# Optimization experiments

Measured on AMD Instinct MI355X. Metric: run time of the kernel, lower is better.

The kernel has to match this reference:

```python
import jax, jax.numpy as jnp
import numpy as np

NUM_HEADS = 8
HEAD_DIM = 64  # hidden_dim // num_heads = 512 // 8
THRESHOLD = 0.5


def setup_inputs() -> dict:
    key = jax.random.key(0)
    ks = jax.random.split(key, 12)
    B, T, D, Hd = 4, 1024, 512, 512
    s = 0.02
    inp = {
        'x': jax.random.normal(ks[0], (B, T, D), dtype=jnp.float32),
        'Wq': jax.random.normal(ks[1], (D, Hd), dtype=jnp.float32) * s,
        'bq': jnp.zeros((Hd,), jnp.float32),
        'Wk': jax.random.normal(ks[2], (D, Hd), dtype=jnp.float32) * s,
        'bk': jnp.zeros((Hd,), jnp.float32),
        'Wv': jax.random.normal(ks[3], (D, Hd), dtype=jnp.float32) * s,
        'bv': jnp.zeros((Hd,), jnp.float32),
        'conv_w': jax.random.normal(ks[4], (NUM_HEADS,), dtype=jnp.float32) * 0.3,
        'conv_b': jnp.zeros((1,), jnp.float32),
        'Wfh': jax.random.normal(ks[5], (Hd, Hd), dtype=jnp.float32) * s,
        'bfh': jnp.zeros((Hd,), jnp.float32),
        'Wfg': jax.random.normal(ks[6], (Hd, Hd), dtype=jnp.float32) * s,
        'bfg': jnp.zeros((Hd,), jnp.float32),
        'Wrh': jax.random.normal(ks[7], (Hd, Hd), dtype=jnp.float32) * s,
        'brh': jnp.zeros((Hd,), jnp.float32),
        'Wrg': jax.random.normal(ks[8], (Hd, Hd), dtype=jnp.float32) * s,
        'brg': jnp.zeros((Hd,), jnp.float32),
    }
    return inp


def reference(x, Wq, bq, Wk, bk, Wv, bv, conv_w, conv_b,
              Wfh, bfh, Wfg, bfg, Wrh, brh, Wrg, brg):
    B, T, D = x.shape
    H, hd = NUM_HEADS, HEAD_DIM
    scale = hd ** -0.5

    q = (x @ Wq + bq).reshape(B, T, H, hd).transpose(0, 2, 1, 3)  # [B,H,T,hd]
    k = (x @ Wk + bk).reshape(B, T, H, hd).transpose(0, 2, 1, 3)
    v = (x @ Wv + bv).reshape(B, T, H, hd).transpose(0, 2, 1, 3)

    scores = jnp.einsum('bhqd,bhkd->bhqk', q, k) * scale        # [B,H,T,T]
    A_t = jax.nn.softmax(scores, axis=-1)

    # cross-head 1x1 conv: weighted sum over heads -> [B,1,T,T]
    R_f = jax.nn.sigmoid(jnp.einsum('bhqk,h->bqk', A_t, conv_w) + conv_b[0])
    R_f = R_f[:, None]                                           # [B,1,T,T]
    M_f = (R_f <= THRESHOLD).astype(A_t.dtype)
    M_r = (1.0 - R_f <= THRESHOLD).astype(A_t.dtype)

    A_f = jax.nn.softmax(A_t * M_f, axis=-1)
    A_r = jax.nn.softmax(A_t * M_r, axis=-1)

    T_f = jnp.einsum('bhqk,bhkd->bhqd', A_f, v).transpose(0, 2, 1, 3).reshape(B, T, H * hd)
    T_r = jnp.einsum('bhqk,bhkd->bhqd', A_r, v).transpose(0, 2, 1, 3).reshape(B, T, H * hd)

    F_f = T_f @ Wfh + bfh
    G_f = jax.nn.sigmoid(T_f @ Wfg + bfg)
    F_r = T_r @ Wrh + brh
    G_r = jax.nn.sigmoid(T_r @ Wrg + brg)

    G_cat = jax.nn.softmax(jnp.stack([G_f, G_r], axis=-1), axis=-1)  # [B,T,Hd,2]
    F_t = F_f * G_cat[..., 0] + F_r * G_cat[..., 1]
    return F_t
```

## Files before the change

### kernel.cpp

```cpp
#include <hip/hip_runtime.h>
#include <hip/hip_bf16.h>
#include <stdint.h>

typedef short bf16x8 __attribute__((ext_vector_type(8)));
typedef float f32x4 __attribute__((ext_vector_type(4)));

__device__ __forceinline__ unsigned short f2bf(float f) {
  union { float f; unsigned int u; } v;
  v.f = f;
  unsigned int u = v.u;
  u = (u + 0x7fffu + ((u >> 16) & 1u)) >> 16;
  return (unsigned short)u;
}

__device__ __forceinline__ unsigned int cvt_pk_bf16(float lo, float hi) {
  unsigned int r;
  asm("v_cvt_pk_bf16_f32 %0, %1, %2" : "=v"(r) : "v"(lo), "v"(hi));
  return r;
}

typedef union { bf16x8 v; unsigned int u[4]; } frag_u;

__device__ __forceinline__ void gload16(const void* g, void* lds) {
  __builtin_amdgcn_global_load_lds(
      (const __attribute__((address_space(1))) unsigned int*)(unsigned long long)g,
      (__attribute__((address_space(3))) unsigned int*)(unsigned long long)(unsigned)(unsigned long long)lds,
      16, 0, 0);
}

__device__ __forceinline__ bf16x8 lds_frag(const unsigned short* t, int row, int ch4q) {
  return *(const bf16x8*)(t + row * 64 + ((ch4q ^ (row & 7)) << 3));
}


__global__ __launch_bounds__(256) void prep_kernel(
    const float* __restrict__ x,
    const float* __restrict__ Wq, const float* __restrict__ Wk, const float* __restrict__ Wv,
    const float* __restrict__ Wfh, const float* __restrict__ Wfg,
    const float* __restrict__ Wrh, const float* __restrict__ Wrg,
    unsigned short* __restrict__ xb, unsigned short* __restrict__ wt) {
  int bid = blockIdx.x;
  int tid = threadIdx.x;
  if (bid < 256) {
    const float4* xi = (const float4*)x;
#pragma unroll
    for (int rep = 0; rep < 8; rep++) {
      int i = bid * 256 + tid + rep * 65536;
      float4 v = xi[i];
      uint2 u;
      u.x = cvt_pk_bf16(v.x, v.y);
      u.y = cvt_pk_bf16(v.z, v.w);
      *(uint2*)&xb[(size_t)i * 4] = u;
    }
  } else {
    __shared__ float tile[64][65];
    int t = bid - 256;
    int mat = t >> 6;
    t &= 63;
    int tr = (t >> 3) * 64, tc = (t & 7) * 64;
    const float* W = (mat == 0) ? Wq : (mat == 1) ? Wk : (mat == 2) ? Wv
                   : (mat == 3) ? Wfh : (mat == 4) ? Wfg : (mat == 5) ? Wrh : Wrg;
    unsigned short* Wt = wt + (size_t)mat * 512 * 512;
    for (int rep = 0; rep < 16; rep++) {
      int idx = rep * 256 + tid;
      int r = idx >> 6, c = idx & 63;
      tile[r][c] = W[(tr + r) * 512 + tc + c];
    }
    __syncthreads();
    for (int rep = 0; rep < 16; rep++) {
      int idx = rep * 256 + tid;
      int r = idx >> 6, c = idx & 63;
      Wt[(tc + r) * 512 + tr + c] = f2bf(tile[c][r]);
    }
  }
}

__global__ __launch_bounds__(256, 2) void qkv_kernel(
    const unsigned short* __restrict__ xb,
    const unsigned short* __restrict__ wtq, const unsigned short* __restrict__ wtk,
    const unsigned short* __restrict__ wtv,
    const float* __restrict__ bq, const float* __restrict__ bk, const float* __restrict__ bv,
    unsigned short* __restrict__ Qfrag, unsigned short* __restrict__ Kfrag,
    unsigned short* __restrict__ Vfrag) {
  __shared__ __attribute__((aligned(16))) unsigned short smem[32768];
  unsigned short* st0 = smem;
  unsigned short* st1 = smem + 4608;
  unsigned short* st2 = smem + 9216;
  const int m0 = blockIdx.y * 64, n0 = blockIdx.x * 64;
  const int tid = threadIdx.x, w = tid >> 6, lane = tid & 63;
  const int c = lane & 15, quad = lane >> 4;
  const int wm = w & 1, wn = w >> 1;
  const int rsel = lane >> 3, csel = lane & 7;
  const int sc = csel ^ rsel;
  const char* Ag  = (const char*)xb  + (size_t)(m0 + w * 16 + rsel) * 1024 + sc * 16;
  const char* Bgq = (const char*)wtq + (size_t)(n0 + w * 16 + rsel) * 1024 + sc * 16;
  const char* Bgk = (const char*)wtk + (size_t)(n0 + w * 16 + rsel) * 1024 + sc * 16;
  const char* Bgv = (const char*)wtv + (size_t)(n0 + w * 16 + rsel) * 1024 + sc * 16;
  const int woff = w * 1024;

  f32x4 acc[3][2][2];
  f32x4 z4 = {0.f, 0.f, 0.f, 0.f};
#pragma unroll
  for (int o = 0; o < 3; o++)
#pragma unroll
    for (int i = 0; i < 2; i++)
#pragma unroll
      for (int j = 0; j < 2; j++) acc[o][i][j] = z4;

  {
    unsigned short* base = smem;
    gload16(Ag, base + woff);              gload16(Ag + 8192, base + woff + 512);
    gload16(Bgq, base + 4096 + woff);      gload16(Bgq + 8192, base + 4096 + woff + 512);
    gload16(Bgk, base + 8192 + woff);      gload16(Bgk + 8192, base + 8192 + woff + 512);
    gload16(Bgv, base + 12288 + woff);     gload16(Bgv + 8192, base + 12288 + woff + 512);
  }
  __syncthreads();

  for (int ks = 0; ks < 8; ks++) {
    unsigned short* cur = smem + (ks & 1) * 16384;
    if (ks < 7) {
      unsigned short* nxt = smem + ((ks + 1) & 1) * 16384;
      const int kb = (ks + 1) * 128;
      gload16(Ag + kb, nxt + woff);          gload16(Ag + kb + 8192, nxt + woff + 512);
      gload16(Bgq + kb, nxt + 4096 + woff);  gload16(Bgq + kb + 8192, nxt + 4096 + woff + 512);
      gload16(Bgk + kb, nxt + 8192 + woff);  gload16(Bgk + kb + 8192, nxt + 8192 + woff + 512);
      gload16(Bgv + kb, nxt + 12288 + woff); gload16(Bgv + kb + 8192, nxt + 12288 + woff + 512);
    }
#pragma unroll
    for (int ch = 0; ch < 2; ch++) {
      const int cq = ch * 4 + quad;
      bf16x8 a0 = lds_frag(cur, wm * 32 + c, cq);
      bf16x8 a1 = lds_frag(cur, wm * 32 + 16 + c, cq);
#pragma unroll
      for (int nt = 0; nt < 2; nt++) {
        const int rb = wn * 32 + nt * 16 + c;
        bf16x8 fq = lds_frag(cur + 4096, rb, cq);
        bf16x8 fk = lds_frag(cur + 8192, rb, cq);
        bf16x8 fv = lds_frag(cur + 12288, rb, cq);
        acc[0][0][nt] = __builtin_amdgcn_mfma_f32_16x16x32_bf16(a0, fq, acc[0][0][nt], 0, 0, 0);
        acc[0][1][nt] = __builtin_amdgcn_mfma_f32_16x16x32_bf16(a1, fq, acc[0][1][nt], 0, 0, 0);
        acc[1][0][nt] = __builtin_amdgcn_mfma_f32_16x16x32_bf16(a0, fk, acc[1][0][nt], 0, 0, 0);
        acc[1][1][nt] = __builtin_amdgcn_mfma_f32_16x16x32_bf16(a1, fk, acc[1][1][nt], 0, 0, 0);
        acc[2][0][nt] = __builtin_amdgcn_mfma_f32_16x16x32_bf16(a0, fv, acc[2][0][nt], 0, 0, 0);
        acc[2][1][nt] = __builtin_amdgcn_mfma_f32_16x16x32_bf16(a1, fv, acc[2][1][nt], 0, 0, 0);
      }
    }
    __syncthreads();
  }

#pragma unroll
  for (int ms = 0; ms < 2; ms++)
#pragma unroll
    for (int nt = 0; nt < 2; nt++) {
      int n_l = wn * 32 + nt * 16 + c;
      int n = n0 + n_l;
      float biasq = bq[n], biask = bk[n], biasv = bv[n];
#pragma unroll
      for (int r = 0; r < 4; r++) {
        int m_l = wm * 32 + ms * 16 + quad * 4 + r;
        st0[m_l * 72 + n_l] = f2bf((acc[0][ms][nt][r] + biasq) * 0.125f);
        st1[m_l * 72 + n_l] = f2bf(acc[1][ms][nt][r] + biask);
        st2[n_l * 72 + m_l] = f2bf(acc[2][ms][nt][r] + biasv);
      }
    }
  __syncthreads();

  {
    const int h = n0 >> 6;
    const int bb = m0 >> 10, t0b = (m0 & 1023) >> 4;
#pragma unroll
    for (int sub = 0; sub < 2; sub++) {
      uint4 vq = *(uint4*)&st0[(w * 16 + c) * 72 + sub * 32 + quad * 8];
      uint4 vk = *(uint4*)&st1[(w * 16 + c) * 72 + sub * 32 + quad * 8];
      size_t base = (size_t)((bb * 64 + t0b + w) * 8192) + h * 1024 + sub * 512 + lane * 8;
      *(uint4*)&Qfrag[base] = vq;
      *(uint4*)&Kfrag[base] = vk;
    }
    const int ktq = t0b + w;
    const int ktp = ktq >> 1, half = ktq & 1;
#pragma unroll
    for (int dm = 0; dm < 4; dm++) {
      uint2 vv = *(uint2*)&st2[(dm * 16 + c) * 72 + w * 16 + quad * 4];
      size_t base = (size_t)(bb * 8 + h) * 65536 + (size_t)(ktp * 4 + dm) * 512
                  + lane * 8 + half * 4;
      *(uint2*)&Vfrag[base] = vv;
    }
  }
}

__global__ __launch_bounds__(512, 2) void attn_kernel(
    const unsigned short* __restrict__ Qfrag, const unsigned short* __restrict__ Kfrag,
    const unsigned short* __restrict__ Vfrag,
    const float* __restrict__ conv_w, const float* __restrict__ conv_b,
    unsigned short* __restrict__ Tfb, unsigned short* __restrict__ Trb) {
  const int b = blockIdx.x, qt = blockIdx.y;
  const int tid = threadIdx.x, w = tid >> 6, lane = tid & 63;
  const int c = lane & 15, quad = lane >> 4;
  __shared__ float zbuf[8][16];
  __shared__ float izbuf[8][16];
  __shared__ __attribute__((aligned(16))) float red[2 * 8 * 4 * 64 * 4];
  __shared__ float zred[2][8][16];

  f32x4 z4 = {0.f, 0.f, 0.f, 0.f};
  const float cb = conv_b[0];
  const size_t qbase = (size_t)((b * 64 + qt) * 8192) + lane * 8;
  const size_t kb0 = (size_t)((b * 64 + w * 8) * 8192) + lane * 8;
  const size_t vb0 = (size_t)(b * 8) * 65536 + lane * 8;

  f32x4 g[8];
#pragma unroll
  for (int j = 0; j < 8; j++) g[j] = {cb, cb, cb, cb};

  for (int h = 0; h < 8; h++) {
    bf16x8 qf0 = *(const bf16x8*)&Qfrag[qbase + h * 1024];
    bf16x8 qf1 = *(const bf16x8*)&Qfrag[qbase + h * 1024 + 512];
    f32x4 p[8];
    float zh = 0.f;
#pragma unroll
    for (int j = 0; j < 8; j++) {
      const size_t kb = kb0 + (size_t)j * 8192 + h * 1024;
      bf16x8 kf0 = *(const bf16x8*)&Kfrag[kb];
      bf16x8 kf1 = *(const bf16x8*)&Kfrag[kb + 512];
      f32x4 s = __builtin_amdgcn_mfma_f32_16x16x32_bf16(kf0, qf0, z4, 0, 0, 0);
      s = __builtin_amdgcn_mfma_f32_16x16x32_bf16(kf1, qf1, s, 0, 0, 0);
      p[j][0] = __expf(s[0]); p[j][1] = __expf(s[1]);
      p[j][2] = __expf(s[2]); p[j][3] = __expf(s[3]);
      zh += (p[j][0] + p[j][1]) + (p[j][2] + p[j][3]);
    }
    zh += __shfl_xor(zh, 16); zh += __shfl_xor(zh, 32);
    __syncthreads();
    if (quad == 0) zbuf[w][c] = zh;
    __syncthreads();
    float Z = ((zbuf[0][c] + zbuf[1][c]) + (zbuf[2][c] + zbuf[3][c]))
            + ((zbuf[4][c] + zbuf[5][c]) + (zbuf[6][c] + zbuf[7][c]));
    const float izq = 1.0f / Z;
    if (w == 0 && quad == 0) izbuf[h][c] = izq;
    const float cwz = conv_w[h] * izq;
#pragma unroll
    for (int j = 0; j < 8; j++) {
      g[j][0] += cwz * p[j][0]; g[j][1] += cwz * p[j][1];
      g[j][2] += cwz * p[j][2]; g[j][3] += cwz * p[j][3];
    }
  }

  unsigned int mmx[4], mmy[4];
#pragma unroll
  for (int t = 0; t < 4; t++) {
    unsigned int p0 = 0, p1 = 0;
#pragma unroll
    for (int r = 0; r < 4; r++) {
      p0 |= ((g[2 * t][r] <= 0.f ? 1u : 0u) | (g[2 * t][r] >= 0.f ? 2u : 0u)) << (8 * r);
      p1 |= ((g[2 * t + 1][r] <= 0.f ? 1u : 0u) | (g[2 * t + 1][r] >= 0.f ? 2u : 0u)) << (8 * r);
    }
    mmx[t] = p0; mmy[t] = p1;
  }
  __syncthreads();

  frag_u ones;
  ones.u[0] = 0x3F803F80u; ones.u[1] = 0x3F803F80u;
  ones.u[2] = 0x3F803F80u; ones.u[3] = 0x3F803F80u;

  const int fr = w >> 2, dmslot = w & 3;
  const size_t tbase = (size_t)(b * 1024 + qt * 16 + c) * 512;
  unsigned short* dstsel = (fr == 0) ? Tfb : Trb;

  for (int h = 0; h < 8; h++) {
    bf16x8 qf0 = *(const bf16x8*)&Qfrag[qbase + h * 1024];
    bf16x8 qf1 = *(const bf16x8*)&Qfrag[qbase + h * 1024 + 512];
    const float iz_h = izbuf[h][c];
    f32x4 accf[4], accr[4];
#pragma unroll
    for (int i = 0; i < 4; i++) { accf[i] = z4; accr[i] = z4; }
    f32x4 zf4 = z4, zr4 = z4;
#pragma unroll
    for (int t = 0; t < 4; t++) {
      const size_t kba = kb0 + (size_t)(2 * t) * 8192 + h * 1024;
      const size_t kbb = kba + 8192;
      bf16x8 ka0 = *(const bf16x8*)&Kfrag[kba];
      bf16x8 ka1 = *(const bf16x8*)&Kfrag[kba + 512];
      bf16x8 kb0f = *(const bf16x8*)&Kfrag[kbb];
      bf16x8 kb1f = *(const bf16x8*)&Kfrag[kbb + 512];
      f32x4 sa = __builtin_amdgcn_mfma_f32_16x16x32_bf16(ka0, qf0, z4, 0, 0, 0);
      sa = __builtin_amdgcn_mfma_f32_16x16x32_bf16(ka1, qf1, sa, 0, 0, 0);
      f32x4 sb = __builtin_amdgcn_mfma_f32_16x16x32_bf16(kb0f, qf0, z4, 0, 0, 0);
      sb = __builtin_amdgcn_mfma_f32_16x16x32_bf16(kb1f, qf1, sb, 0, 0, 0);
      float ea[4], eb[4];
#pragma unroll
      for (int r = 0; r < 4; r++) {
        ea[r] = __expf(__expf(sa[r]) * iz_h);
        eb[r] = __expf(__expf(sb[r]) * iz_h);
      }
      frag_u pF, pR;
      pF.u[0] = cvt_pk_bf16((mmx[t] & 0x1u)       ? ea[0] : 1.f, (mmx[t] & 0x100u)     ? ea[1] : 1.f);
      pF.u[1] = cvt_pk_bf16((mmx[t] & 0x10000u)   ? ea[2] : 1.f, (mmx[t] & 0x1000000u) ? ea[3] : 1.f);
      pF.u[2] = cvt_pk_bf16((mmy[t] & 0x1u)       ? eb[0] : 1.f, (mmy[t] & 0x100u)     ? eb[1] : 1.f);
      pF.u[3] = cvt_pk_bf16((mmy[t] & 0x10000u)   ? eb[2] : 1.f, (mmy[t] & 0x1000000u) ? eb[3] : 1.f);
      pR.u[0] = cvt_pk_bf16((mmx[t] & 0x2u)       ? ea[0] : 1.f, (mmx[t] & 0x200u)     ? ea[1] : 1.f);
      pR.u[1] = cvt_pk_bf16((mmx[t] & 0x20000u)   ? ea[2] : 1.f, (mmx[t] & 0x2000000u) ? ea[3] : 1.f);
      pR.u[2] = cvt_pk_bf16((mmy[t] & 0x2u)       ? eb[0] : 1.f, (mmy[t] & 0x200u)     ? eb[1] : 1.f);
      pR.u[3] = cvt_pk_bf16((mmy[t] & 0x20000u)   ? eb[2] : 1.f, (mmy[t] & 0x2000000u) ? eb[3] : 1.f);
      zf4 = __builtin_amdgcn_mfma_f32_16x16x32_bf16(ones.v, pF.v, zf4, 0, 0, 0);
      zr4 = __builtin_amdgcn_mfma_f32_16x16x32_bf16(ones.v, pR.v, zr4, 0, 0, 0);
      const size_t vbh = vb0 + (size_t)h * 65536 + (size_t)((w * 4 + t) * 4) * 512;
#pragma unroll
      for (int dm = 0; dm < 4; dm++) {
        bf16x8 vf = *(const bf16x8*)&Vfrag[vbh + (size_t)dm * 512];
        accf[dm] = __builtin_amdgcn_mfma_f32_16x16x32_bf16(vf, pF.v, accf[dm], 0, 0, 0);
        accr[dm] = __builtin_amdgcn_mfma_f32_16x16x32_bf16(vf, pR.v, accr[dm], 0, 0, 0);
      }
    }
    __syncthreads();
#pragma unroll
    for (int dm = 0; dm < 4; dm++) {
      *(f32x4*)&red[(((0 * 8 + w) * 4 + dm) * 64 + lane) * 4] = accf[dm];
      *(f32x4*)&red[(((1 * 8 + w) * 4 + dm) * 64 + lane) * 4] = accr[dm];
    }
    if (quad == 0) { zred[0][w][c] = zf4[0]; zred[1][w][c] = zr4[0]; }
    __syncthreads();
    {
      f32x4 o = z4;
#pragma unroll
      for (int w2 = 0; w2 < 8; w2++)
        o += *(const f32x4*)&red[(((fr * 8 + w2) * 4 + dmslot) * 64 + lane) * 4];
      float Zq = 0.f;
#pragma unroll
      for (int w2 = 0; w2 < 8; w2++) Zq += zred[fr][w2][c];
      const float iz = 1.0f / Zq;
      uint2 u;
      u.x = cvt_pk_bf16(o[0] * iz, o[1] * iz);
      u.y = cvt_pk_bf16(o[2] * iz, o[3] * iz);
      *(uint2*)&dstsel[tbase + h * 64 + dmslot * 16 + quad * 4] = u;
    }
  }
}

__global__ __launch_bounds__(256, 4) void final_kernel(
    const unsigned short* __restrict__ Tfb, const unsigned short* __restrict__ Trb,
    const unsigned short* __restrict__ wfh, const unsigned short* __restrict__ wfg,
    const unsigned short* __restrict__ wrh, const unsigned short* __restrict__ wrg,
    const float* __restrict__ bfh, const float* __restrict__ bfg,
    const float* __restrict__ brh, const float* __restrict__ brg,
    float* __restrict__ out) {
  __shared__ __attribute__((aligned(16))) unsigned short smem[16384];
  const int m0 = blockIdx.y * 64, n0 = blockIdx.x * 32;
  const int tid = threadIdx.x, w = tid >> 6, lane = tid & 63;
  const int c = lane & 15, quad = lane >> 4;
  const int wm = w & 1, wn = w >> 1;
  const int rsel = lane >> 3, csel = lane & 7;
  const int sc = csel ^ rsel;
  const char* Agf = (const char*)Tfb + (size_t)(m0 + w * 16 + rsel) * 1024 + sc * 16;
  const char* Agr = (const char*)Trb + (size_t)(m0 + w * 16 + rsel) * 1024 + sc * 16;
  const char* Bg0 = (const char*)wfh + (size_t)(n0 + w * 8 + rsel) * 1024 + sc * 16;
  const char* Bg1 = (const char*)wfg + (size_t)(n0 + w * 8 + rsel) * 1024 + sc * 16;
  const char* Bg2 = (const char*)wrh + (size_t)(n0 + w * 8 + rsel) * 1024 + sc * 16;
  const char* Bg3 = (const char*)wrg + (size_t)(n0 + w * 8 + rsel) * 1024 + sc * 16;
  unsigned short* lAf = smem + w * 1024;
  unsigned short* lAr = smem + 4096 + w * 1024;
  unsigned short* l0 = smem + 8192 + w * 512;
  unsigned short* l1 = smem + 10240 + w * 512;
  unsigned short* l2 = smem + 12288 + w * 512;
  unsigned short* l3 = smem + 14336 + w * 512;

  f32x4 acc[4][2];
  f32x4 z4 = {0.f, 0.f, 0.f, 0.f};
#pragma unroll
  for (int o = 0; o < 4; o++)
#pragma unroll
    for (int m = 0; m < 2; m++) acc[o][m] = z4;

  for (int ks = 0; ks < 8; ks++) {
    if (ks) __syncthreads();
    const int kb = ks * 128;
    gload16(Agf + kb, lAf);  gload16(Agf + kb + 8192, lAf + 512);
    gload16(Agr + kb, lAr);  gload16(Agr + kb + 8192, lAr + 512);
    gload16(Bg0 + kb, l0);
    gload16(Bg1 + kb, l1);
    gload16(Bg2 + kb, l2);
    gload16(Bg3 + kb, l3);
    __syncthreads();
#pragma unroll
    for (int ch = 0; ch < 2; ch++) {
      const int cq = ch * 4 + quad;
      bf16x8 af0 = lds_frag(smem, wm * 32 + c, cq);
      bf16x8 af1 = lds_frag(smem, wm * 32 + 16 + c, cq);
      bf16x8 ar0 = lds_frag(smem + 4096, wm * 32 + c, cq);
      bf16x8 ar1 = lds_frag(smem + 4096, wm * 32 + 16 + c, cq);
      const int rb = wn * 16 + c;
      bf16x8 f0 = lds_frag(smem + 8192, rb, cq);
      bf16x8 f1 = lds_frag(smem + 10240, rb, cq);
      bf16x8 f2 = lds_frag(smem + 12288, rb, cq);
      bf16x8 f3 = lds_frag(smem + 14336, rb, cq);
      acc[0][0] = __builtin_amdgcn_mfma_f32_16x16x32_bf16(af0, f0, acc[0][0], 0, 0, 0);
      acc[0][1] = __builtin_amdgcn_mfma_f32_16x16x32_bf16(af1, f0, acc[0][1], 0, 0, 0);
      acc[1][0] = __builtin_amdgcn_mfma_f32_16x16x32_bf16(af0, f1, acc[1][0], 0, 0, 0);
      acc[1][1] = __builtin_amdgcn_mfma_f32_16x16x32_bf16(af1, f1, acc[1][1], 0, 0, 0);
      acc[2][0] = __builtin_amdgcn_mfma_f32_16x16x32_bf16(ar0, f2, acc[2][0], 0, 0, 0);
      acc[2][1] = __builtin_amdgcn_mfma_f32_16x16x32_bf16(ar1, f2, acc[2][1], 0, 0, 0);
      acc[3][0] = __builtin_amdgcn_mfma_f32_16x16x32_bf16(ar0, f3, acc[3][0], 0, 0, 0);
      acc[3][1] = __builtin_amdgcn_mfma_f32_16x16x32_bf16(ar1, f3, acc[3][1], 0, 0, 0);
    }
  }

  {
    int n = n0 + wn * 16 + c;
    float b0 = bfh[n], b1 = bfg[n], b2 = brh[n], b3 = brg[n];
#pragma unroll
    for (int m = 0; m < 2; m++) {
      int t0 = m0 + wm * 32 + m * 16 + quad * 4;
#pragma unroll
      for (int r = 0; r < 4; r++) {
        int t = t0 + r;
        float Ff = acc[0][m][r] + b0;
        float Gf = 1.0f / (1.0f + __expf(-(acc[1][m][r] + b1)));
        float Fr = acc[2][m][r] + b2;
        float Gr = 1.0f / (1.0f + __expf(-(acc[3][m][r] + b3)));
        float ef = __expf(Gf), er = __expf(Gr);
        out[(size_t)t * 512 + n] = (Ff * ef + Fr * er) / (ef + er);
      }
    }
  }
}

extern "C" void kernel_launch(void* const* d_in, const int* in_sizes, int n_in,
                              void* d_out, int out_size, void* d_ws, size_t ws_size,
                              hipStream_t stream) {
  const float* x   = (const float*)d_in[0];
  const float* Wq  = (const float*)d_in[1];
  const float* bq  = (const float*)d_in[2];
  const float* Wk  = (const float*)d_in[3];
  const float* bk  = (const float*)d_in[4];
  const float* Wv  = (const float*)d_in[5];
  const float* bv  = (const float*)d_in[6];
  const float* cw  = (const float*)d_in[7];
  const float* cb  = (const float*)d_in[8];
  const float* Wfh = (const float*)d_in[9];
  const float* bfh = (const float*)d_in[10];
  const float* Wfg = (const float*)d_in[11];
  const float* bfg = (const float*)d_in[12];
  const float* Wrh = (const float*)d_in[13];
  const float* brh = (const float*)d_in[14];
  const float* Wrg = (const float*)d_in[15];
  const float* brg = (const float*)d_in[16];

  char* ws = (char*)d_ws;
  const size_t MB = 1024 * 1024;
  unsigned short* xb    = (unsigned short*)(ws + 0 * MB);
  unsigned short* Qfrag = (unsigned short*)(ws + 4 * MB);
  unsigned short* Kfrag = (unsigned short*)(ws + 8 * MB);
  unsigned short* Vfrag = (unsigned short*)(ws + 12 * MB);
  unsigned short* Tfb   = (unsigned short*)(ws + 16 * MB);
  unsigned short* Trb   = (unsigned short*)(ws + 20 * MB);
  unsigned short* wt    = (unsigned short*)(ws + 24 * MB);
  const size_t WSZ = 512 * 512;

  prep_kernel<<<704, 256, 0, stream>>>(x, Wq, Wk, Wv, Wfh, Wfg, Wrh, Wrg, xb, wt);
  qkv_kernel<<<dim3(8, 64), 256, 0, stream>>>(xb, wt + 0 * WSZ, wt + 1 * WSZ, wt + 2 * WSZ,
                                              bq, bk, bv, Qfrag, Kfrag, Vfrag);
  attn_kernel<<<dim3(4, 64), 512, 0, stream>>>(Qfrag, Kfrag, Vfrag, cw, cb, Tfb, Trb);
  final_kernel<<<dim3(16, 64), 256, 0, stream>>>(Tfb, Trb, wt + 3 * WSZ, wt + 4 * WSZ,
                                                 wt + 5 * WSZ, wt + 6 * WSZ,
                                                 bfh, bfg, brh, brg, (float*)d_out);
}
```

Before: 171.9 us.

## Halve QKV GEMM M-tile and drop LDS double buffering for higher occupancy

The QKV projection kernel now uses 32-row M tiles instead of 64, doubling the grid to 1024 blocks. It drops the double-buffered LDS prefetch for a single buffer with load-sync-compute stages, shrinking shared memory and raising the launch-bounds occupancy hint from 2 to 4. The epilogue repacking is reworked so each wave handles part of the smaller tile. The intent is more parallelism and latency hiding across the GPU; in exchange, memory-to-compute overlap inside a block is lost and the weight tiles are reloaded twice as often.

```diff
diff --git a/kernel.cpp b/kernel.cpp
--- a/kernel.cpp
+++ b/kernel.cpp
@@ -75,115 +75,103 @@
   }
 }
 
-__global__ __launch_bounds__(256, 2) void qkv_kernel(
+__global__ __launch_bounds__(256, 4) void qkv_kernel(
     const unsigned short* __restrict__ xb,
     const unsigned short* __restrict__ wtq, const unsigned short* __restrict__ wtk,
     const unsigned short* __restrict__ wtv,
     const float* __restrict__ bq, const float* __restrict__ bk, const float* __restrict__ bv,
     unsigned short* __restrict__ Qfrag, unsigned short* __restrict__ Kfrag,
     unsigned short* __restrict__ Vfrag) {
-  __shared__ __attribute__((aligned(16))) unsigned short smem[32768];
+  __shared__ __attribute__((aligned(16))) unsigned short smem[14336];
+  unsigned short* As = smem;
+  unsigned short* Bq = smem + 2048;
+  unsigned short* Bk = smem + 6144;
+  unsigned short* Bv = smem + 10240;
   unsigned short* st0 = smem;
-  unsigned short* st1 = smem + 4608;
-  unsigned short* st2 = smem + 9216;
-  const int m0 = blockIdx.y * 64, n0 = blockIdx.x * 64;
+  unsigned short* st1 = smem + 2304;
+  unsigned short* st2 = smem + 4608;
+  const int m0 = blockIdx.y * 32, n0 = blockIdx.x * 64;
   const int tid = threadIdx.x, w = tid >> 6, lane = tid & 63;
   const int c = lane & 15, quad = lane >> 4;
   const int wm = w & 1, wn = w >> 1;
   const int rsel = lane >> 3, csel = lane & 7;
   const int sc = csel ^ rsel;
-  const char* Ag  = (const char*)xb  + (size_t)(m0 + w * 16 + rsel) * 1024 + sc * 16;
+  const char* Ag  = (const char*)xb  + (size_t)(m0 + w * 8 + rsel) * 1024 + sc * 16;
   const char* Bgq = (const char*)wtq + (size_t)(n0 + w * 16 + rsel) * 1024 + sc * 16;
   const char* Bgk = (const char*)wtk + (size_t)(n0 + w * 16 + rsel) * 1024 + sc * 16;
   const char* Bgv = (const char*)wtv + (size_t)(n0 + w * 16 + rsel) * 1024 + sc * 16;
-  const int woff = w * 1024;
-
-  f32x4 acc[3][2][2];
+  unsigned short* lA = As + w * 512;
+  unsigned short* lQ = Bq + w * 1024;
+  unsigned short* lK = Bk + w * 1024;
+  unsigned short* lV = Bv + w * 1024;
+
+  f32x4 acc[3][2];
   f32x4 z4 = {0.f, 0.f, 0.f, 0.f};
 #pragma unroll
   for (int o = 0; o < 3; o++)
 #pragma unroll
-    for (int i = 0; i < 2; i++)
-#pragma unroll
-      for (int j = 0; j < 2; j++) acc[o][i][j] = z4;
-
-  {
-    unsigned short* base = smem;
-    gload16(Ag, base + woff);              gload16(Ag + 8192, base + woff + 512);
-    gload16(Bgq, base + 4096 + woff);      gload16(Bgq + 8192, base + 4096 + woff + 512);
-    gload16(Bgk, base + 8192 + woff);      gload16(Bgk + 8192, base + 8192 + woff + 512);
-    gload16(Bgv, base + 12288 + woff);     gload16(Bgv + 8192, base + 12288 + woff + 512);
-  }
-  __syncthreads();
+    for (int j = 0; j < 2; j++) acc[o][j] = z4;
 
   for (int ks = 0; ks < 8; ks++) {
-    unsigned short* cur = smem + (ks & 1) * 16384;
-    if (ks < 7) {
-      unsigned short* nxt = smem + ((ks + 1) & 1) * 16384;
-      const int kb = (ks + 1) * 128;
-      gload16(Ag + kb, nxt + woff);          gload16(Ag + kb + 8192, nxt + woff + 512);
-      gload16(Bgq + kb, nxt + 4096 + woff);  gload16(Bgq + kb + 8192, nxt + 4096 + woff + 512);
-      gload16(Bgk + kb, nxt + 8192 + woff);  gload16(Bgk + kb + 8192, nxt + 8192 + woff + 512);
-      gload16(Bgv + kb, nxt + 12288 + woff); gload16(Bgv + kb + 8192, nxt + 12288 + woff + 512);
-    }
+    if (ks) __syncthreads();
+    const int kb = ks * 128;
+    gload16(Ag + kb, lA);
+    gload16(Bgq + kb, lQ);  gload16(Bgq + kb + 8192, lQ + 512);
+    gload16(Bgk + kb, lK);  gload16(Bgk + kb + 8192, lK + 512);
+    gload16(Bgv + kb, lV);  gload16(Bgv + kb + 8192, lV + 512);
+    __syncthreads();
 #pragma unroll
     for (int ch = 0; ch < 2; ch++) {
       const int cq = ch * 4 + quad;
-      bf16x8 a0 = lds_frag(cur, wm * 32 + c, cq);
-      bf16x8 a1 = lds_frag(cur, wm * 32 + 16 + c, cq);
+      bf16x8 a = lds_frag(As, wm * 16 + c, cq);
 #pragma unroll
       for (int nt = 0; nt < 2; nt++) {
         const int rb = wn * 32 + nt * 16 + c;
-        bf16x8 fq = lds_frag(cur + 4096, rb, cq);
-        bf16x8 fk = lds_frag(cur + 8192, rb, cq);
-        bf16x8 fv = lds_frag(cur + 12288, rb, cq);
-        acc[0][0][nt] = __builtin_amdgcn_mfma_f32_16x16x32_bf16(a0, fq, acc[0][0][nt], 0, 0, 0);
-        acc[0][1][nt] = __builtin_amdgcn_mfma_f32_16x16x32_bf16(a1, fq, acc[0][1][nt], 0, 0, 0);
-        acc[1][0][nt] = __builtin_amdgcn_mfma_f32_16x16x32_bf16(a0, fk, acc[1][0][nt], 0, 0, 0);
-        acc[1][1][nt] = __builtin_amdgcn_mfma_f32_16x16x32_bf16(a1, fk, acc[1][1][nt], 0, 0, 0);
-        acc[2][0][nt] = __builtin_amdgcn_mfma_f32_16x16x32_bf16(a0, fv, acc[2][0][nt], 0, 0, 0);
-        acc[2][1][nt] = __builtin_amdgcn_mfma_f32_16x16x32_bf16(a1, fv, acc[2][1][nt], 0, 0, 0);
+        bf16x8 fq = lds_frag(Bq, rb, cq);
+        bf16x8 fk = lds_frag(Bk, rb, cq);
+        bf16x8 fv = lds_frag(Bv, rb, cq);
+        acc[0][nt] = __builtin_amdgcn_mfma_f32_16x16x32_bf16(a, fq, acc[0][nt], 0, 0, 0);
+        acc[1][nt] = __builtin_amdgcn_mfma_f32_16x16x32_bf16(a, fk, acc[1][nt], 0, 0, 0);
+        acc[2][nt] = __builtin_amdgcn_mfma_f32_16x16x32_bf16(a, fv, acc[2][nt], 0, 0, 0);
       }
     }
-    __syncthreads();
-  }
-
-#pragma unroll
-  for (int ms = 0; ms < 2; ms++)
-#pragma unroll
-    for (int nt = 0; nt < 2; nt++) {
-      int n_l = wn * 32 + nt * 16 + c;
-      int n = n0 + n_l;
-      float biasq = bq[n], biask = bk[n], biasv = bv[n];
-#pragma unroll
-      for (int r = 0; r < 4; r++) {
-        int m_l = wm * 32 + ms * 16 + quad * 4 + r;
-        st0[m_l * 72 + n_l] = f2bf((acc[0][ms][nt][r] + biasq) * 0.125f);
-        st1[m_l * 72 + n_l] = f2bf(acc[1][ms][nt][r] + biask);
-        st2[n_l * 72 + m_l] = f2bf(acc[2][ms][nt][r] + biasv);
-      }
-    }
+  }
+  __syncthreads();
+
+#pragma unroll
+  for (int nt = 0; nt < 2; nt++) {
+    int n_l = wn * 32 + nt * 16 + c;
+    int n = n0 + n_l;
+    float biasq = bq[n], biask = bk[n], biasv = bv[n];
+#pragma unroll
+    for (int r = 0; r < 4; r++) {
+      int m_l = wm * 16 + quad * 4 + r;
+      st0[m_l * 72 + n_l] = f2bf((acc[0][nt][r] + biasq) * 0.125f);
+      st1[m_l * 72 + n_l] = f2bf(acc[1][nt][r] + biask);
+      st2[n_l * 40 + m_l] = f2bf(acc[2][nt][r] + biasv);
+    }
+  }
   __syncthreads();
 
   {
     const int h = n0 >> 6;
     const int bb = m0 >> 10, t0b = (m0 & 1023) >> 4;
-#pragma unroll
-    for (int sub = 0; sub < 2; sub++) {
-      uint4 vq = *(uint4*)&st0[(w * 16 + c) * 72 + sub * 32 + quad * 8];
-      uint4 vk = *(uint4*)&st1[(w * 16 + c) * 72 + sub * 32 + quad * 8];
-      size_t base = (size_t)((bb * 64 + t0b + w) * 8192) + h * 1024 + sub * 512 + lane * 8;
-      *(uint4*)&Qfrag[base] = vq;
-      *(uint4*)&Kfrag[base] = vk;
-    }
-    const int ktq = t0b + w;
+    const int tw = w >> 1, sub = w & 1;
+    uint4 vq = *(uint4*)&st0[(tw * 16 + c) * 72 + sub * 32 + quad * 8];
+    uint4 vk = *(uint4*)&st1[(tw * 16 + c) * 72 + sub * 32 + quad * 8];
+    size_t base = (size_t)((bb * 64 + t0b + tw) * 8192) + h * 1024 + sub * 512 + lane * 8;
+    *(uint4*)&Qfrag[base] = vq;
+    *(uint4*)&Kfrag[base] = vk;
+    const int tv = w & 1;
+    const int ktq = t0b + tv;
     const int ktp = ktq >> 1, half = ktq & 1;
 #pragma unroll
-    for (int dm = 0; dm < 4; dm++) {
-      uint2 vv = *(uint2*)&st2[(dm * 16 + c) * 72 + w * 16 + quad * 4];
-      size_t base = (size_t)(bb * 8 + h) * 65536 + (size_t)(ktp * 4 + dm) * 512
-                  + lane * 8 + half * 4;
-      *(uint2*)&Vfrag[base] = vv;
+    for (int dmj = 0; dmj < 2; dmj++) {
+      const int dm = (w >> 1) * 2 + dmj;
+      uint2 vv = *(uint2*)&st2[(dm * 16 + c) * 40 + tv * 16 + quad * 4];
+      size_t vbase = (size_t)(bb * 8 + h) * 65536 + (size_t)(ktp * 4 + dm) * 512
+                   + lane * 8 + half * 4;
+      *(uint2*)&Vfrag[vbase] = vv;
     }
   }
 }
@@ -454,8 +442,8 @@
   const size_t WSZ = 512 * 512;
 
   prep_kernel<<<704, 256, 0, stream>>>(x, Wq, Wk, Wv, Wfh, Wfg, Wrh, Wrg, xb, wt);
-  qkv_kernel<<<dim3(8, 64), 256, 0, stream>>>(xb, wt + 0 * WSZ, wt + 1 * WSZ, wt + 2 * WSZ,
-                                              bq, bk, bv, Qfrag, Kfrag, Vfrag);
+  qkv_kernel<<<dim3(8, 128), 256, 0, stream>>>(xb, wt + 0 * WSZ, wt + 1 * WSZ, wt + 2 * WSZ,
+                                               bq, bk, bv, Qfrag, Kfrag, Vfrag);
   attn_kernel<<<dim3(4, 64), 512, 0, stream>>>(Qfrag, Kfrag, Vfrag, cw, cb, Tfb, Trb);
   final_kernel<<<dim3(16, 64), 256, 0, stream>>>(Tfb, Trb, wt + 3 * WSZ, wt + 4 * WSZ,
                                                  wt + 5 * WSZ, wt + 6 * WSZ,
```

Result: no change. 175.3 us (+2.0%).
